# Performance work log

Measured on AMD Instinct MI355X. Metric: run time of the kernel, lower is better.

The kernel has to match this reference:

```python
import jax, jax.numpy as jnp
import numpy as np
from jax import lax

S, B, C = 7, 2, 20
W, H = 448.0, 448.0
IOU_THR = 0.1
PROB_THR = 8e-25
BATCH = 16
L = S * S * C + S * S * B + S * S * B * 4  # 1470
N = S * S * B * C                          # 1960 (box,class) candidates per image


def setup_inputs() -> dict:
    key = jax.random.key(0)
    prediction = jax.random.uniform(key, (BATCH, L), dtype=jnp.float32)
    return {"prediction": prediction}


def _pairwise_iou(b):
    # b: [N,4] boxes as (x_center, y_center, w, h); faithful to YoloDetector.iou
    x, y, w, h = b[:, 0], b[:, 1], b[:, 2], b[:, 3]
    tb = (jnp.minimum(x[:, None] + 0.5 * w[:, None], x[None, :] + 0.5 * w[None, :])
          - jnp.maximum(x[:, None] - 0.5 * w[:, None], x[None, :] - 0.5 * w[None, :]))
    lr = (jnp.minimum(y[:, None] + 0.5 * h[:, None], y[None, :] + 0.5 * h[None, :])
          - jnp.maximum(y[:, None] - 0.5 * h[:, None], y[None, :] - 0.5 * h[None, :]))
    inter = jnp.where((tb < 0) | (lr < 0), 0.0, tb * lr)
    area = w * h
    return inter / (area[:, None] + area[None, :] - inter)


def _decode_one(pred):
    # split flat prediction as in traDim(mode=3)
    SC, SB = S * S * C, S * S * B
    class_prob = pred[:SC].reshape(S, S, C)
    confidence = pred[SC:SC + SB].reshape(S, S, B)
    boxes = pred[SC + SB:].reshape(S, S, B, 4)

    # grid offsets: boxes[...,0] += row index i, boxes[...,1] += col index j
    idx = jnp.arange(S, dtype=pred.dtype)
    x = (boxes[..., 0] + idx[:, None, None]) / S * W
    y = (boxes[..., 1] + idx[None, :, None]) / S * H
    w = boxes[..., 2] * boxes[..., 2] * W
    h = boxes[..., 3] * boxes[..., 3] * H
    boxes_xywh = jnp.stack([x, y, w, h], axis=-1)          # [S,S,B,4]

    # eProbs[i,j,b,c] = classProb[i,j,c] * confidence[i,j,b]
    e_probs = class_prob[:, :, None, :] * confidence[:, :, :, None]  # [S,S,B,C]
    mask = e_probs >= PROB_THR
    # original uses argmax over the boolean mask along class axis for the class id
    cls = jnp.argmax(mask, axis=3)                         # [S,S,B]

    # flatten all (cell, box, class) candidates; below-threshold probs -> 0 (masking
    # replaces the data-dependent boolean filtering of the original)
    probs = jnp.where(mask, e_probs, 0.0).reshape(-1)                          # [N]
    boxes_c = jnp.broadcast_to(boxes_xywh[:, :, :, None, :], (S, S, B, C, 4)).reshape(-1, 4)
    cls_c = jnp.broadcast_to(cls[:, :, :, None], (S, S, B, C)).reshape(-1)     # [N]

    order = jnp.argsort(-probs)                            # descending by prob
    probs = probs[order]
    boxes_c = boxes_c[order]
    cls_c = cls_c[order]

    iou = _pairwise_iou(boxes_c)                           # [N,N], memory-dominant

    def step(p, xs):
        row, i = xs
        pivot = p[i]
        sup = (jnp.arange(N) > i) & (row > IOU_THR) & (pivot > 0)
        return jnp.where(sup, 0.0, p), None

    probs_nms, _ = lax.scan(step, probs, (iou, jnp.arange(N)))
    return boxes_c, probs_nms, cls_c


def reference(prediction):
    # returns (boxes [BATCH,N,4], probs_after_nms [BATCH,N], class_ids [BATCH,N]);
    # suppressed / sub-threshold candidates carry prob == 0 (fixed-shape analogue of
    # the original's boolean filtering)
    return jax.vmap(_decode_one)(prediction)
```

## Files before the change

### kernel.cpp

```cpp
#include <hip/hip_runtime.h>


constexpr int S_  = 7;
constexpr int Cc  = 20;
constexpr int NBOX  = 98;
constexpr int NENT  = 1960;
constexpr int NPAD  = 2048;
constexpr int LPRED = 1470;
constexpr int BATCH = 16;
constexpr float IOU_THR_  = 0.1f;
constexpr float PROB_THR_ = 8e-25f;

__device__ __forceinline__ unsigned long long rl64(unsigned long long v, int l)
{
    unsigned lo = (unsigned)__builtin_amdgcn_readlane((int)(unsigned)v, l);
    unsigned hi = (unsigned)__builtin_amdgcn_readlane((int)(unsigned)(v >> 32), l);
    return ((unsigned long long)hi << 32) | lo;
}

__global__ __launch_bounds__(1024)
void yolo_nms_kernel(const float* __restrict__ pred_all, float* __restrict__ out)
{
    const int b    = blockIdx.x;
    const int tid  = threadIdx.x;
    const int wv   = tid >> 6, lane = tid & 63;
    const unsigned long long lt = (1ull << lane) - 1ull;
    const unsigned long long le = lt | (1ull << lane);
    const float* pred = pred_all + b * LPRED;

    __shared__ float s_pred[LPRED];
    __shared__ unsigned int   sProb[2][NPAD];
    __shared__ unsigned short sIdx [2][NPAD];
    __shared__ alignas(16) unsigned short sHist[2][16 * 256];
    __shared__ unsigned int   sTot[256];
    __shared__ float bXh[NBOX], bXl[NBOX], bYh[NBOX], bYl[NBOX], bA[NBOX];
    __shared__ float4 bBox[NBOX];
    __shared__ int   bCls[NBOX];
    __shared__ unsigned long long iouRow[NBOX * 2];
    __shared__ int firstpos[NBOX], boxorder[NBOX], kept[NBOX], s_nvalid;

    for (int i = tid; i < LPRED; i += 1024) s_pred[i] = pred[i];
    reinterpret_cast<unsigned long long*>(sHist[0])[tid] = 0ull;
    if (tid == 0) s_nvalid = 0;
    if (tid < NBOX) { kept[tid] = 0; firstpos[tid] = 0x7FFFFFFF; }
    __syncthreads();

    if (tid < NBOX) {
        const int bo = tid, cell = bo >> 1;
        const int ci = cell / S_, cj = cell % S_;
        const float bx = s_pred[1078 + bo * 4 + 0];
        const float by = s_pred[1078 + bo * 4 + 1];
        const float bw = s_pred[1078 + bo * 4 + 2];
        const float bh = s_pred[1078 + bo * 4 + 3];
        const float x = (bx + (float)ci) / 7.0f * 448.0f;
        const float y = (by + (float)cj) / 7.0f * 448.0f;
        const float w = bw * bw * 448.0f;
        const float h = bh * bh * 448.0f;
        bBox[bo] = make_float4(x, y, w, h);
        bXh[bo] = x + 0.5f * w;  bXl[bo] = x - 0.5f * w;
        bYh[bo] = y + 0.5f * h;  bYl[bo] = y - 0.5f * h;
        bA[bo]  = w * h;
        const float conf = s_pred[980 + bo];
        int cls = 0;
        for (int c = 0; c < Cc; ++c)
            if (s_pred[cell * Cc + c] * conf >= PROB_THR_) { cls = c; break; }
        bCls[bo] = cls;
    }

    #pragma unroll
    for (int s = 0; s < 2; ++s) {
        const int e = 2 * tid + s;
        unsigned pb = 0u;
        if (e < NENT) {
            const int bo = e / Cc, c = e - bo * Cc, cell = bo >> 1;
            const float ep = s_pred[cell * Cc + c] * s_pred[980 + bo];
            if (ep >= PROB_THR_) pb = __float_as_uint(ep);
        }
        sProb[0][e] = pb;
        sIdx[0][e]  = (unsigned short)e;
    }
    __syncthreads();

    for (int r = wv; r < NBOX; r += 16) {
        const float rXh = bXh[r], rXl = bXl[r], rYh = bYh[r], rYl = bYl[r], rA = bA[r];
        bool s1 = false, s2 = false;
        {
            const int j = lane;
            const float tb = fminf(rXh, bXh[j]) - fmaxf(rXl, bXl[j]);
            const float lr = fminf(rYh, bYh[j]) - fmaxf(rYl, bYl[j]);
            const float inter = (tb < 0.0f || lr < 0.0f) ? 0.0f : tb * lr;
            const float iou = inter / (rA + bA[j] - inter);
            s1 = (iou > IOU_THR_);
        }
        if (lane + 64 < NBOX) {
            const int j = lane + 64;
            const float tb = fminf(rXh, bXh[j]) - fmaxf(rXl, bXl[j]);
            const float lr = fminf(rYh, bYh[j]) - fmaxf(rYl, bYl[j]);
            const float inter = (tb < 0.0f || lr < 0.0f) ? 0.0f : tb * lr;
            const float iou = inter / (rA + bA[j] - inter);
            s2 = (iou > IOU_THR_);
        }
        const unsigned long long m1 = __ballot(s1);
        const unsigned long long m2 = __ballot(s2);
        if (lane == 0) { iouRow[r * 2] = m1; iouRow[r * 2 + 1] = m2; }
    }

    int src = 0;
    #pragma unroll
    for (int pass = 0; pass < 4; ++pass) {
        const int hb  = pass & 1;
        const int dst = src ^ 1;
        const int sh  = pass * 8;

        const unsigned q0 = sProb[src][2 * tid];
        const unsigned q1 = sProb[src][2 * tid + 1];
        const unsigned short j0 = sIdx[src][2 * tid];
        const unsigned short j1 = sIdx[src][2 * tid + 1];
        const unsigned d0 = 0xFFu ^ ((q0 >> sh) & 0xFFu);
        const unsigned d1 = 0xFFu ^ ((q1 >> sh) & 0xFFu);

        unsigned long long mAA = ~0ull, mAB = ~0ull, mBA = ~0ull, mBB = ~0ull;
        #pragma unroll
        for (int bit = 0; bit < 8; ++bit) {
            const unsigned long long ba = __ballot((d0 >> bit) & 1u);
            const unsigned long long bb = __ballot((d1 >> bit) & 1u);
            mAA &= ((d0 >> bit) & 1u) ? ba : ~ba;
            mAB &= ((d0 >> bit) & 1u) ? bb : ~bb;
            mBA &= ((d1 >> bit) & 1u) ? ba : ~ba;
            mBB &= ((d1 >> bit) & 1u) ? bb : ~bb;
        }
        const int rank0 = __popcll(mAA & lt) + __popcll(mAB & lt);
        const int rank1 = __popcll(mBA & le) + __popcll(mBB & lt);
        sHist[hb][wv * 256 + d0] = (unsigned short)(__popcll(mAA) + __popcll(mAB));
        sHist[hb][wv * 256 + d1] = (unsigned short)(__popcll(mBA) + __popcll(mBB));
        __syncthreads();

        if (tid < 256) {
            unsigned run = 0;
            unsigned short pf[16];
            #pragma unroll
            for (int w = 0; w < 16; ++w) {
                const unsigned c = sHist[hb][w * 256 + tid];
                pf[w] = (unsigned short)run;
                run += c;
            }
            #pragma unroll
            for (int w = 0; w < 16; ++w) sHist[hb][w * 256 + tid] = pf[w];
            sTot[tid] = run;
        }
        __syncthreads();

        if (wv == 0) {
            const unsigned v0 = sTot[4 * lane],     v1 = sTot[4 * lane + 1];
            const unsigned v2 = sTot[4 * lane + 2], v3 = sTot[4 * lane + 3];
            const unsigned sm = v0 + v1 + v2 + v3;
            unsigned inc = sm;
            #pragma unroll
            for (int off = 1; off < 64; off <<= 1) {
                const unsigned t = __shfl_up(inc, off, 64);
                if (lane >= off) inc += t;
            }
            const unsigned ex = inc - sm;
            sTot[4 * lane]     = ex;
            sTot[4 * lane + 1] = ex + v0;
            sTot[4 * lane + 2] = ex + v0 + v1;
            sTot[4 * lane + 3] = ex + v0 + v1 + v2;
        }
        __syncthreads();

        const unsigned pos0 = sTot[d0] + sHist[hb][wv * 256 + d0] + (unsigned)rank0;
        const unsigned pos1 = sTot[d1] + sHist[hb][wv * 256 + d1] + (unsigned)rank1;
        sProb[dst][pos0] = q0;  sIdx[dst][pos0] = j0;
        sProb[dst][pos1] = q1;  sIdx[dst][pos1] = j1;
        if (pass == 3) {
            if (q0) atomicMin(&firstpos[j0 / Cc], (int)pos0);
            if (q1) atomicMin(&firstpos[j1 / Cc], (int)pos1);
        } else {
            reinterpret_cast<unsigned long long*>(sHist[hb ^ 1])[tid] = 0ull;
        }
        __syncthreads();
        src = dst;
    }

    if (tid < NBOX) {
        const int fp = firstpos[tid];
        if (fp != 0x7FFFFFFF) {
            int r = 0;
            for (int b2 = 0; b2 < NBOX; ++b2) r += (firstpos[b2] < fp) ? 1 : 0;
            boxorder[r] = tid;
            atomicAdd(&s_nvalid, 1);
        }
    }
    __syncthreads();

    if (tid < 64) {
        const int nv = s_nvalid;
        int bb0 = -1, bb1 = -1;
        unsigned long long r00 = 0, r01 = 0, r10 = 0, r11 = 0;
        if (tid < nv) {
            bb0 = boxorder[tid];
            r00 = iouRow[bb0 * 2]; r01 = iouRow[bb0 * 2 + 1];
        }
        if (tid + 64 < nv) {
            bb1 = boxorder[tid + 64];
            r10 = iouRow[bb1 * 2]; r11 = iouRow[bb1 * 2 + 1];
        }
        unsigned long long sup0 = 0, sup1 = 0, k0 = 0, k1 = 0;
        for (int r = 0; r < nv; ++r) {
            int bb; unsigned long long rw0, rw1;
            if (r < 64) {
                bb  = __builtin_amdgcn_readlane(bb0, r);
                rw0 = rl64(r00, r); rw1 = rl64(r01, r);
            } else {
                bb  = __builtin_amdgcn_readlane(bb1, r - 64);
                rw0 = rl64(r10, r - 64); rw1 = rl64(r11, r - 64);
            }
            const bool supped = (bb < 64) ? ((sup0 >> bb) & 1ull)
                                          : ((sup1 >> (bb - 64)) & 1ull);
            if (!supped) {
                if (bb < 64) k0 |= 1ull << bb; else k1 |= 1ull << (bb - 64);
                sup0 |= rw0; sup1 |= rw1;
            }
        }
        kept[tid] = (int)((k0 >> tid) & 1ull);
        if (tid < NBOX - 64) kept[tid + 64] = (int)((k1 >> tid) & 1ull);
    }
    __syncthreads();

    float* outBoxes = out + b * (NENT * 4);
    float* outProbs = out + BATCH * NENT * 4 + b * NENT;
    float* outCls   = out + BATCH * NENT * 5 + b * NENT;
    if (tid < NENT / 2) {
        #pragma unroll
        for (int s = 0; s < 2; ++s) {
            const int kp = 2 * tid + s;
            const unsigned q = sProb[0][kp];
            const int j  = sIdx[0][kp];
            const int bo = j / Cc;
            *reinterpret_cast<float4*>(outBoxes + kp * 4) = bBox[bo];
            outProbs[kp] = (q != 0u && kp == firstpos[bo] && kept[bo])
                             ? __uint_as_float(q) : 0.0f;
            outCls[kp] = (float)bCls[bo];
        }
    }
}

extern "C" void kernel_launch(void* const* d_in, const int* in_sizes, int n_in,
                              void* d_out, int out_size, void* d_ws, size_t ws_size,
                              hipStream_t stream)
{
    const float* pred = (const float*)d_in[0];
    float* out = (float*)d_out;
    yolo_nms_kernel<<<BATCH, 1024, 0, stream>>>(pred, out);
}
```

Before: 32.58 us.

## Scatter boxes and classes directly from final radix pass, sparse prob writes

```diff
diff --git a/kernel.cpp b/kernel.cpp
--- a/kernel.cpp
+++ b/kernel.cpp
@@ -28,6 +28,10 @@
     const unsigned long long le = lt | (1ull << lane);
     const float* pred = pred_all + b * LPRED;
 
+    float* outBoxes = out + b * (NENT * 4);
+    float* outProbs = out + BATCH * NENT * 4 + b * NENT;
+    float* outCls   = out + BATCH * NENT * 5 + b * NENT;
+
     __shared__ float s_pred[LPRED];
     __shared__ unsigned int   sProb[2][NPAD];
     __shared__ unsigned short sIdx [2][NPAD];
@@ -35,10 +39,14 @@
     __shared__ unsigned int   sTot[256];
     __shared__ float bXh[NBOX], bXl[NBOX], bYh[NBOX], bYl[NBOX], bA[NBOX];
     __shared__ float4 bBox[NBOX];
-    __shared__ int   bCls[NBOX];
+    __shared__ float bClsF[NBOX], bPmax[NBOX];
     __shared__ unsigned long long iouRow[NBOX * 2];
     __shared__ int firstpos[NBOX], boxorder[NBOX], kept[NBOX], s_nvalid;
 
+    {
+        float4* zp = reinterpret_cast<float4*>(outProbs);
+        if (tid < NENT / 4) zp[tid] = make_float4(0.f, 0.f, 0.f, 0.f);
+    }
     for (int i = tid; i < LPRED; i += 1024) s_pred[i] = pred[i];
     reinterpret_cast<unsigned long long*>(sHist[0])[tid] = 0ull;
     if (tid == 0) s_nvalid = 0;
@@ -61,10 +69,15 @@
         bYh[bo] = y + 0.5f * h;  bYl[bo] = y - 0.5f * h;
         bA[bo]  = w * h;
         const float conf = s_pred[980 + bo];
-        int cls = 0;
-        for (int c = 0; c < Cc; ++c)
-            if (s_pred[cell * Cc + c] * conf >= PROB_THR_) { cls = c; break; }
-        bCls[bo] = cls;
+        unsigned mask = 0u; float pm = 0.f;
+        #pragma unroll
+        for (int c = 0; c < Cc; ++c) {
+            const float ep = s_pred[cell * Cc + c] * conf;
+            if (ep >= PROB_THR_) mask |= 1u << c;
+            pm = fmaxf(pm, ep);
+        }
+        bClsF[bo] = (float)(mask ? (__ffs(mask) - 1) : 0);
+        bPmax[bo] = pm;
     }
 
     #pragma unroll
@@ -170,13 +183,24 @@
 
         const unsigned pos0 = sTot[d0] + sHist[hb][wv * 256 + d0] + (unsigned)rank0;
         const unsigned pos1 = sTot[d1] + sHist[hb][wv * 256 + d1] + (unsigned)rank1;
-        sProb[dst][pos0] = q0;  sIdx[dst][pos0] = j0;
-        sProb[dst][pos1] = q1;  sIdx[dst][pos1] = j1;
-        if (pass == 3) {
-            if (q0) atomicMin(&firstpos[j0 / Cc], (int)pos0);
-            if (q1) atomicMin(&firstpos[j1 / Cc], (int)pos1);
+
+        if (pass < 3) {
+            sProb[dst][pos0] = q0;  sIdx[dst][pos0] = j0;
+            sProb[dst][pos1] = q1;  sIdx[dst][pos1] = j1;
+            reinterpret_cast<unsigned long long*>(sHist[hb ^ 1])[tid] = 0ull;
         } else {
-            reinterpret_cast<unsigned long long*>(sHist[hb ^ 1])[tid] = 0ull;
+            if (j0 < NENT) {
+                const int bo = j0 / Cc;
+                *reinterpret_cast<float4*>(outBoxes + pos0 * 4) = bBox[bo];
+                outCls[pos0] = bClsF[bo];
+                if (q0) atomicMin(&firstpos[bo], (int)pos0);
+            }
+            if (j1 < NENT) {
+                const int bo = j1 / Cc;
+                *reinterpret_cast<float4*>(outBoxes + pos1 * 4) = bBox[bo];
+                outCls[pos1] = bClsF[bo];
+                if (q1) atomicMin(&firstpos[bo], (int)pos1);
+            }
         }
         __syncthreads();
         src = dst;
@@ -227,22 +251,7 @@
     }
     __syncthreads();
 
-    float* outBoxes = out + b * (NENT * 4);
-    float* outProbs = out + BATCH * NENT * 4 + b * NENT;
-    float* outCls   = out + BATCH * NENT * 5 + b * NENT;
-    if (tid < NENT / 2) {
-        #pragma unroll
-        for (int s = 0; s < 2; ++s) {
-            const int kp = 2 * tid + s;
-            const unsigned q = sProb[0][kp];
-            const int j  = sIdx[0][kp];
-            const int bo = j / Cc;
-            *reinterpret_cast<float4*>(outBoxes + kp * 4) = bBox[bo];
-            outProbs[kp] = (q != 0u && kp == firstpos[bo] && kept[bo])
-                             ? __uint_as_float(q) : 0.0f;
-            outCls[kp] = (float)bCls[bo];
-        }
-    }
+    if (tid < NBOX && kept[tid]) outProbs[firstpos[tid]] = bPmax[tid];
 }
 
 extern "C" void kernel_launch(void* const* d_in, const int* in_sizes, int n_in,
```

Result: no change. 31.99 us (-1.8%).
